# Optimization experiments

Measured on AMD Instinct MI355X. Metric: run time of the kernel, lower is better.

The kernel has to match this reference:

```python
import jax, jax.numpy as jnp
import numpy as np

H = 2048          # hidden size
NH = 32           # query heads
NKV = 8           # kv heads
HD = H // NH      # head dim = 64
GROUPS = NH // NKV
S = 2048          # seq len
B = 1
SCALE = HD ** -0.5


def _rope_tables(seq, dim, base=10000.0):
    inv = 1.0 / (base ** (np.arange(0, dim, 2, dtype=np.float32) / dim))
    t = np.arange(seq, dtype=np.float32)
    freqs = np.outer(t, inv)                     # [S, dim/2]
    emb = np.concatenate([freqs, freqs], axis=-1)  # [S, dim]
    return jnp.asarray(np.cos(emb)), jnp.asarray(np.sin(emb))


def setup_inputs() -> dict:
    key = jax.random.key(0)
    ks = jax.random.split(key, 5)
    x = jax.random.normal(ks[0], (B, S, H), dtype=jnp.float32)
    wq = jax.random.normal(ks[1], (H, NH * HD), dtype=jnp.float32) * (H ** -0.5)
    wk = jax.random.normal(ks[2], (H, NKV * HD), dtype=jnp.float32) * (H ** -0.5)
    wv = jax.random.normal(ks[3], (H, NKV * HD), dtype=jnp.float32) * (H ** -0.5)
    wo = jax.random.normal(ks[4], (NH * HD, H), dtype=jnp.float32) * (H ** -0.5)
    cos, sin = _rope_tables(S, HD)
    mask = jnp.tril(jnp.ones((S, S), dtype=bool))[None, None]  # causal [1,1,S,S]
    return {"x": x, "wq": wq, "wk": wk, "wv": wv, "wo": wo,
            "cos": cos, "sin": sin, "mask": mask}


def _rotate_half(t):
    t1, t2 = jnp.split(t, 2, axis=-1)
    return jnp.concatenate([-t2, t1], axis=-1)


def reference(x, wq, wk, wv, wo, cos, sin, mask):
    b, s, _ = x.shape
    # projections
    q = (x @ wq).reshape(b, s, NH, HD).transpose(0, 2, 1, 3)    # [B,NH,S,HD]
    k = (x @ wk).reshape(b, s, NKV, HD).transpose(0, 2, 1, 3)   # [B,NKV,S,HD]
    v = (x @ wv).reshape(b, s, NKV, HD).transpose(0, 2, 1, 3)
    # RoPE (cos/sin broadcast over batch and heads)
    c = cos[None, None]; sn = sin[None, None]
    q = q * c + _rotate_half(q) * sn
    k = k * c + _rotate_half(k) * sn
    # GQA: repeat kv heads to match query heads
    k = jnp.repeat(k, GROUPS, axis=1)                           # [B,NH,S,HD]
    v = jnp.repeat(v, GROUPS, axis=1)
    # scores + causal mask + softmax (dropout p=0 -> identity in eval)
    scores = SCALE * jnp.einsum('bhqd,bhkd->bhqk', q, k)
    scores = jnp.where(mask, scores, -jnp.inf)
    attn = jax.nn.softmax(scores, axis=-1)
    out = jnp.einsum('bhqk,bhkd->bhqd', attn, v)
    out = out.transpose(0, 2, 1, 3).reshape(b, s, NH * HD)
    return out @ wo
```

## Files before the change

### kernel.cpp

```cpp
#include <hip/hip_runtime.h>

typedef unsigned short u16;
typedef unsigned u32;
typedef u16 u16x8 __attribute__((ext_vector_type(8)));
typedef u16 u16x4 __attribute__((ext_vector_type(4)));
typedef u32 u32x4 __attribute__((ext_vector_type(4)));
typedef __bf16 bf8 __attribute__((ext_vector_type(8)));
typedef float f32x4 __attribute__((ext_vector_type(4)));
typedef float f32x16 __attribute__((ext_vector_type(16)));

__device__ __forceinline__ u16 f2b(float f) {
  unsigned u = __float_as_uint(f);
  u += 0x7FFFu + ((u >> 16) & 1u);
  return (u16)(u >> 16);
}
__device__ __forceinline__ float b2f(u16 h) {
  return __uint_as_float(((unsigned)h) << 16);
}
__device__ __forceinline__ bf8 asbf8(u16x8 v) {
  return __builtin_bit_cast(bf8, v);
}
__device__ __forceinline__ void gll16(const u16* g, u16* l) {
  __builtin_amdgcn_global_load_lds(
      (const __attribute__((address_space(1))) unsigned*)(g),
      (__attribute__((address_space(3))) unsigned*)(l), 16, 0, 0);
}
__device__ __forceinline__ u32 cvtpk(float lo, float hi) {
  u32 r;
  asm("v_cvt_pk_bf16_f32 %0, %1, %2" : "=v"(r) : "v"(lo), "v"(hi));
  return r;
}
__device__ __forceinline__ void plswap(u32& a, u32& b) {
  asm("v_permlane32_swap_b32 %0, %1" : "+v"(a), "+v"(b));
}
__device__ __forceinline__ float ex2(float x) {
  return __builtin_amdgcn_exp2f(x);
}
#define MFMA32(A,B,C) __builtin_amdgcn_mfma_f32_32x32x16_bf16(A,B,C,0,0,0)


__global__ __launch_bounds__(256) void xconv(const float* __restrict__ x,
                                             u16* __restrict__ xb) {
  int i = (blockIdx.x * 256 + threadIdx.x) * 4;
  float4 v = *(const float4*)(x + i);
  u16x4 o;
  o[0] = f2b(v.x); o[1] = f2b(v.y); o[2] = f2b(v.z); o[3] = f2b(v.w);
  *(u16x4*)(xb + i) = o;
}

__global__ __launch_bounds__(256) void wtrans(const float* __restrict__ in,
                                              u16* __restrict__ out,
                                              int N, int K) {
  __shared__ float tile[32][33];
  int tx = threadIdx.x & 31, ty = threadIdx.x >> 5;
  int n0 = blockIdx.x * 32, k0 = blockIdx.y * 32;
#pragma unroll
  for (int yy = 0; yy < 32; yy += 8)
    tile[ty + yy][tx] = in[(size_t)(k0 + ty + yy) * N + n0 + tx];
  __syncthreads();
#pragma unroll
  for (int yy = 0; yy < 32; yy += 8)
    out[(size_t)(n0 + ty + yy) * K + k0 + tx] = f2b(tile[tx][ty + yy]);
}

__global__ __launch_bounds__(256) void reduce_qkv(u16* __restrict__ p0,
                                                  const u16* __restrict__ p1,
                                                  const float* __restrict__ cs,
                                                  const float* __restrict__ sn) {
  int idx = blockIdx.x * 256 + threadIdx.x;
  int s = idx / 384, c8 = (idx % 384) * 8;
  size_t base = (size_t)s * 3072 + c8;
  if (c8 < 2560) {
    int hc = c8 & 63;
    if (hc >= 32) return;
    u16x8 a0 = *(const u16x8*)(p0 + base);
    u16x8 a1 = *(const u16x8*)(p1 + base);
    u16x8 b0 = *(const u16x8*)(p0 + base + 32);
    u16x8 b1 = *(const u16x8*)(p1 + base + 32);
    u16x8 oa, ob;
#pragma unroll
    for (int e = 0; e < 8; ++e) {
      float va = b2f(a0[e]) + b2f(a1[e]);
      float vb = b2f(b0[e]) + b2f(b1[e]);
      float c1 = cs[s * 64 + hc + e],      s1 = sn[s * 64 + hc + e];
      float c2 = cs[s * 64 + hc + 32 + e], s2 = sn[s * 64 + hc + 32 + e];
      oa[e] = f2b(va * c1 - vb * s1);
      ob[e] = f2b(vb * c2 + va * s2);
    }
    *(u16x8*)(p0 + base)      = oa;
    *(u16x8*)(p0 + base + 32) = ob;
  } else {
    u16x8 a0 = *(const u16x8*)(p0 + base);
    u16x8 a1 = *(const u16x8*)(p1 + base);
    u16x8 o;
#pragma unroll
    for (int e = 0; e < 8; ++e) o[e] = f2b(b2f(a0[e]) + b2f(a1[e]));
    *(u16x8*)(p0 + base) = o;
  }
}

__global__ __launch_bounds__(256) void reduce_out(const u16* __restrict__ p0,
                                                  const u16* __restrict__ p1,
                                                  float* __restrict__ out) {
  int idx = blockIdx.x * 256 + threadIdx.x;
  size_t base = (size_t)idx * 8;
  u16x8 a0 = *(const u16x8*)(p0 + base);
  u16x8 a1 = *(const u16x8*)(p1 + base);
  float4 lo, hi;
  lo.x = b2f(a0[0]) + b2f(a1[0]); lo.y = b2f(a0[1]) + b2f(a1[1]);
  lo.z = b2f(a0[2]) + b2f(a1[2]); lo.w = b2f(a0[3]) + b2f(a1[3]);
  hi.x = b2f(a0[4]) + b2f(a1[4]); hi.y = b2f(a0[5]) + b2f(a1[5]);
  hi.z = b2f(a0[6]) + b2f(a1[6]); hi.w = b2f(a0[7]) + b2f(a1[7]);
  *(float4*)(out + base)     = lo;
  *(float4*)(out + base + 4) = hi;
}

__global__ __launch_bounds__(256) void ktrans_f(const u16* __restrict__ qkv,
                                                u16* __restrict__ Kf) {
  int tid = blockIdx.x * 256 + threadIdx.x;
  int s = tid >> 6, cc = tid & 63;
  int kh = cc >> 3, c = cc & 7;
  int j = c >> 1, hi = c & 1;
  int b = s >> 5, la = s & 31;
  u16x8 v = *(const u16x8*)(qkv + (size_t)s * 3072 + 2048 + cc * 8);
  *(u16x8*)(Kf + ((((size_t)(kh * 64 + b) * 4 + j) * 2 + hi) * 32 + la) * 8) = v;
}

__global__ __launch_bounds__(256) void vtrans_f(const u16* __restrict__ qkv,
                                                u16* __restrict__ Vf) {
  int tid = blockIdx.x * 256 + threadIdx.x;
  int s = tid >> 6, cc = tid & 63;
  int kh = cc >> 3, c = cc & 7;
  int m = c >> 2, laB = (c & 3) * 8;
  int b = s >> 5, s5 = s & 31;
  int jj = s5 >> 4, hi = (s5 >> 3) & 1, e = s5 & 7;
  u16x8 v = *(const u16x8*)(qkv + (size_t)s * 3072 + 2560 + cc * 8);
  u16* dst = Vf + (((size_t)(kh * 64 + b) * 4 + m * 2 + jj) * 64 + hi * 32 + laB) * 8 + e;
#pragma unroll
  for (int i = 0; i < 8; ++i) dst[i * 8] = v[i];
}


__global__ __launch_bounds__(256) void gemm_sk(const u16* __restrict__ A,
                                               const u16* __restrict__ Bt,
                                               u16* __restrict__ C0,
                                               u16* __restrict__ C1,
                                               int N, int Kfull, int KH) {
  __shared__ __align__(16) u16 As[128 * 64];
  __shared__ __align__(16) u16 Bs[128 * 64];
  const int t = threadIdx.x;
  const int lane = t & 63, wid = t >> 6;
  const int wm = (wid >> 1) * 64, wn = (wid & 1) * 64;
  const int la = lane & 15, lg = lane >> 4;
  const int m0 = blockIdx.y * 128, n0 = blockIdx.x * 128;
  const int kbeg = blockIdx.z * KH;
  u16* C = blockIdx.z ? C1 : C0;

  const int srow0 = wid * 32 + (lane >> 3);
  const int scolsw = (((lane & 7) ^ (lane >> 3))) * 8;
  const u16* Ap = A + (size_t)(m0 + srow0) * Kfull + kbeg + scolsw;
  const u16* Bp = Bt + (size_t)(n0 + srow0) * Kfull + kbeg + scolsw;
  u16* Adst = &As[wid * 2048];
  u16* Bdst = &Bs[wid * 2048];
  const size_t rstep8 = (size_t)8 * Kfull;

  f32x4 acc[4][4] = {};

  for (int k0 = 0; k0 < KH; k0 += 64) {
    __syncthreads();
#pragma unroll
    for (int cc = 0; cc < 4; ++cc)
      gll16(Ap + k0 + cc * rstep8, Adst + cc * 512);
#pragma unroll
    for (int cc = 0; cc < 4; ++cc)
      gll16(Bp + k0 + cc * rstep8, Bdst + cc * 512);
    __syncthreads();
#pragma unroll
    for (int kk = 0; kk < 2; ++kk) {
      bf8 af[4], bfr[4];
#pragma unroll
      for (int i = 0; i < 4; ++i) {
        const int row = wm + i * 16 + la;
        const int c8 = (kk * 4 + lg) ^ (row & 7);
        af[i] = asbf8(*(const u16x8*)(&As[row * 64 + c8 * 8]));
      }
#pragma unroll
      for (int j = 0; j < 4; ++j) {
        const int row = wn + j * 16 + la;
        const int c8 = (kk * 4 + lg) ^ (row & 7);
        bfr[j] = asbf8(*(const u16x8*)(&Bs[row * 64 + c8 * 8]));
      }
      __builtin_amdgcn_s_setprio(1);
#pragma unroll
      for (int i = 0; i < 4; ++i)
#pragma unroll
        for (int j = 0; j < 4; ++j)
          acc[i][j] = __builtin_amdgcn_mfma_f32_16x16x32_bf16(af[i], bfr[j],
                                                              acc[i][j], 0, 0, 0);
      __builtin_amdgcn_s_setprio(0);
    }
  }

#pragma unroll
  for (int i = 0; i < 4; ++i)
#pragma unroll
    for (int j = 0; j < 4; ++j)
#pragma unroll
      for (int r = 0; r < 4; ++r) {
        int row = m0 + wm + i * 16 + lg * 4 + r;
        int col = n0 + wn + j * 16 + la;
        C[(size_t)row * N + col] = f2b(acc[i][j][r]);
      }
}


#define STEPL(buf, bb) do {                                          \
    const u16* p_ = &smem[(((h2) << 1) | (buf)) * 4096 + lane8];     \
    bf8 K0 = asbf8(*(const u16x8*)(p_));                             \
    bf8 K1 = asbf8(*(const u16x8*)(p_ + 512));                       \
    bf8 K2 = asbf8(*(const u16x8*)(p_ + 1024));                      \
    bf8 K3 = asbf8(*(const u16x8*)(p_ + 1536));                      \
    bf8 V0 = asbf8(*(const u16x8*)(p_ + 2048));                      \
    bf8 V1 = asbf8(*(const u16x8*)(p_ + 2560));                      \
    bf8 V2 = asbf8(*(const u16x8*)(p_ + 3072));                      \
    bf8 V3 = asbf8(*(const u16x8*)(p_ + 3584));                      \
    f32x16 s = {};                                                   \
    __builtin_amdgcn_s_setprio(1);                                   \
    s = MFMA32(K0, qf0, s);                                          \
    s = MFMA32(K1, qf1, s);                                          \
    s = MFMA32(K2, qf2, s);                                          \
    s = MFMA32(K3, qf3, s);                                          \
    __builtin_amdgcn_s_setprio(0);                                   \
    if ((bb) == kmax) {                                              \
      _Pragma("unroll") for (int r = 0; r < 16; ++r) {               \
        int kvr = (bb) * 32 + (r & 3) + 8 * (r >> 2) + 4 * hi;       \
        if (kvr > q0w + la) s[r] = -1e30f;                           \
      }                                                              \
    }                                                                \
    _Pragma("unroll") for (int r = 0; r < 16; ++r)                   \
      s[r] = ex2(s[r] - 32.0f);                                      \
    float z0 = s[0] + s[1],   z1 = s[2] + s[3];                      \
    float z2 = s[4] + s[5],   z3 = s[6] + s[7];                      \
    float z4 = s[8] + s[9],   z5 = s[10] + s[11];                    \
    float z6 = s[12] + s[13], z7 = s[14] + s[15];                    \
    l_run += ((z0 + z1) + (z2 + z3)) + ((z4 + z5) + (z6 + z7));      \
    u32 c0 = cvtpk(s[0], s[1]),   c1 = cvtpk(s[2], s[3]);            \
    u32 c2 = cvtpk(s[4], s[5]),   c3 = cvtpk(s[6], s[7]);            \
    u32 c4 = cvtpk(s[8], s[9]),   c5 = cvtpk(s[10], s[11]);          \
    u32 c6 = cvtpk(s[12], s[13]), c7 = cvtpk(s[14], s[15]);          \
    plswap(c0, c2); plswap(c1, c3); plswap(c4, c6); plswap(c5, c7);  \
    u32x4 t0; t0[0] = c0; t0[1] = c1; t0[2] = c2; t0[3] = c3;        \
    u32x4 t1; t1[0] = c4; t1[1] = c5; t1[2] = c6; t1[3] = c7;        \
    bf8 pa0 = __builtin_bit_cast(bf8, t0);                           \
    bf8 pa1 = __builtin_bit_cast(bf8, t1);                           \
    __builtin_amdgcn_s_setprio(1);                                   \
    o0 = MFMA32(pa0, V0, o0);                                        \
    o0 = MFMA32(pa1, V1, o0);                                        \
    o1 = MFMA32(pa0, V2, o1);                                        \
    o1 = MFMA32(pa1, V3, o1);                                        \
    __builtin_amdgcn_s_setprio(0);                                   \
  } while (0)

#define STG(bb, buf) do {                                            \
    u16* d_ = &smem[((((h2) << 1) | (buf)) * 4096) + sub * 512];     \
    gll16(Kg + (size_t)(bb) * 2048 + sub * 512 + lane8, d_);         \
    gll16(Vg + (size_t)(bb) * 2048 + sub * 512 + lane8, d_ + 2048);  \
  } while (0)

__global__ __launch_bounds__(512, 4) void attn_fwd(const u16* __restrict__ qkv,
                                                   const u16* __restrict__ Kf,
                                                   const u16* __restrict__ Vf,
                                                   u16* __restrict__ aout) {
  const int head = blockIdx.x;
  const int qb = 15 - (int)blockIdx.y;
  const int Q0 = qb * 128;
  const int Kb = qb * 4;
  const int nb = Kb + 4;
  const int ha = nb >> 1;
  const int kh = head >> 2;
  const int t = threadIdx.x;
  const int w = t >> 6, lane = t & 63;
  const int h2 = w >> 2;
  const int wq = w & 3;
  const int sub = wq;
  const int la = lane & 31;
  const int hi = lane >> 5;
  const int lane8 = lane * 8;
  const int q0w = Q0 + 32 * wq;
  const int kmax = Kb + wq;

  __shared__ __align__(16) u16 smem[18432];
  __shared__ float lM[8][32];

  bf8 qf0, qf1, qf2, qf3;
  {
    const u16* qp = qkv + (size_t)(q0w + la) * 3072 + head * 64 + hi * 8;
    const float SC = 0.125f * 1.44269504088896340736f;
#define QLOAD(dst, kk) do {                                          \
      u16x8 v = *(const u16x8*)(qp + (kk) * 16);                     \
      u16x8 sv;                                                      \
      _Pragma("unroll") for (int e = 0; e < 8; ++e)                  \
        sv[e] = f2b(b2f(v[e]) * SC);                                 \
      dst = asbf8(sv);                                               \
    } while (0)
    QLOAD(qf0, 0); QLOAD(qf1, 1); QLOAD(qf2, 2); QLOAD(qf3, 3);
#undef QLOAD
  }

  const u16* Kg = Kf + (size_t)kh * 131072;
  const u16* Vg = Vf + (size_t)kh * 131072;

  f32x16 o0 = {}, o1 = {};
  float l_run = 0.f;

  STG(h2 ? ha : 0, 0);
  __syncthreads();

  for (int i = 0; i < ha; ++i) {
    if (i + 1 < ha) STG(h2 ? (ha + i + 1) : (i + 1), (i + 1) & 1);
    const int bb = h2 ? (ha + i) : i;
    if (bb <= kmax) STEPL(i & 1, bb);
    __syncthreads();
  }

  {
    float lt = l_run + __shfl_xor(l_run, 32);
    if (lane < 32) lM[w][lane] = lt;
#pragma unroll
    for (int r = 0; r < 16; ++r) {
      int crow = (r & 3) + 8 * (r >> 2) + 4 * hi;
      smem[(w * 32 + crow) * 72 + la]      = f2b(o0[r]);
      smem[(w * 32 + crow) * 72 + la + 32] = f2b(o1[r]);
    }
  }
  __syncthreads();

#pragma unroll
  for (int it = 0; it < 2; ++it) {
    const int id = t + it * 512;
    const int q = id >> 3, d0 = (id & 7) * 8;
    const int wA = q >> 5, crow = q & 31;
    float inv = 1.0f / (lM[wA][crow] + lM[wA + 4][crow]);
    u16x8 a = *(const u16x8*)&smem[((wA)     * 32 + crow) * 72 + d0];
    u16x8 b = *(const u16x8*)&smem[((wA + 4) * 32 + crow) * 72 + d0];
    u16x8 outv;
#pragma unroll
    for (int j = 0; j < 8; ++j)
      outv[j] = f2b((b2f(a[j]) + b2f(b[j])) * inv);
    *(u16x8*)(aout + (size_t)(Q0 + q) * 2048 + head * 64 + d0) = outv;
  }
}


extern "C" void kernel_launch(void* const* d_in, const int* in_sizes, int n_in,
                              void* d_out, int out_size, void* d_ws, size_t ws_size,
                              hipStream_t stream) {
  (void)in_sizes; (void)n_in; (void)out_size; (void)ws_size;
  const float* x  = (const float*)d_in[0];
  const float* wq = (const float*)d_in[1];
  const float* wk = (const float*)d_in[2];
  const float* wv = (const float*)d_in[3];
  const float* wo = (const float*)d_in[4];
  const float* cs = (const float*)d_in[5];
  const float* sn = (const float*)d_in[6];

  u16* ws    = (u16*)d_ws;
  u16* xb    = ws;
  u16* wqkvT = ws + 4194304;
  u16* qkv   = ws + 10485760;
  u16* woT   = ws + 16777216;
  u16* ext   = ws + 20971520;
  u16* Kf    = wqkvT;
  u16* Vf    = wqkvT + 1048576;
  u16* aout  = xb;
  u16* op0   = qkv;
  u16* op1   = ext;

  xconv<<<4096, 256, 0, stream>>>(x, xb);
  wtrans<<<dim3(64, 64), 256, 0, stream>>>(wq, wqkvT, 2048, 2048);
  wtrans<<<dim3(16, 64), 256, 0, stream>>>(wk, wqkvT + (size_t)2048 * 2048, 512, 2048);
  wtrans<<<dim3(16, 64), 256, 0, stream>>>(wv, wqkvT + (size_t)2560 * 2048, 512, 2048);
  wtrans<<<dim3(64, 64), 256, 0, stream>>>(wo, woT, 2048, 2048);

  gemm_sk<<<dim3(24, 16, 2), 256, 0, stream>>>(xb, wqkvT, qkv, ext, 3072, 2048, 1024);
  reduce_qkv<<<3072, 256, 0, stream>>>(qkv, ext, cs, sn);
  ktrans_f<<<512, 256, 0, stream>>>(qkv, Kf);
  vtrans_f<<<512, 256, 0, stream>>>(qkv, Vf);
  attn_fwd<<<dim3(32, 16), 512, 0, stream>>>(qkv, Kf, Vf, aout);
  gemm_sk<<<dim3(16, 16, 2), 256, 0, stream>>>(aout, woT, op0, op1, 2048, 2048, 1024);
  reduce_out<<<2048, 256, 0, stream>>>(op0, op1, (float*)d_out);
}
```

Measured before the change: 142.6 us.

## Shrink attention blocks to 64 query rows and merge K/V transpose kernels

The attention kernel now gives each workgroup 64 query rows with 4 waves instead of 128 rows with 8 waves. This doubles the grid to 1024 blocks, which should improve load balance across the causal triangle and raise occupancy. Each wave now issues twice as many global-to-LDS loads per K/V stage. The separate K and V transpose kernels are also merged into one launch to cut launch overhead. In exchange, K/V tiles are reused across fewer query rows, so more global traffic goes to K/V.

```diff
diff --git a/kernel.cpp b/kernel.cpp
--- a/kernel.cpp
+++ b/kernel.cpp
@@ -115,29 +115,30 @@
   *(float4*)(out + base + 4) = hi;
 }
 
-__global__ __launch_bounds__(256) void ktrans_f(const u16* __restrict__ qkv,
-                                                u16* __restrict__ Kf) {
-  int tid = blockIdx.x * 256 + threadIdx.x;
-  int s = tid >> 6, cc = tid & 63;
-  int kh = cc >> 3, c = cc & 7;
-  int j = c >> 1, hi = c & 1;
-  int b = s >> 5, la = s & 31;
-  u16x8 v = *(const u16x8*)(qkv + (size_t)s * 3072 + 2048 + cc * 8);
-  *(u16x8*)(Kf + ((((size_t)(kh * 64 + b) * 4 + j) * 2 + hi) * 32 + la) * 8) = v;
-}
-
-__global__ __launch_bounds__(256) void vtrans_f(const u16* __restrict__ qkv,
-                                                u16* __restrict__ Vf) {
-  int tid = blockIdx.x * 256 + threadIdx.x;
-  int s = tid >> 6, cc = tid & 63;
-  int kh = cc >> 3, c = cc & 7;
-  int m = c >> 2, laB = (c & 3) * 8;
-  int b = s >> 5, s5 = s & 31;
-  int jj = s5 >> 4, hi = (s5 >> 3) & 1, e = s5 & 7;
-  u16x8 v = *(const u16x8*)(qkv + (size_t)s * 3072 + 2560 + cc * 8);
-  u16* dst = Vf + (((size_t)(kh * 64 + b) * 4 + m * 2 + jj) * 64 + hi * 32 + laB) * 8 + e;
-#pragma unroll
-  for (int i = 0; i < 8; ++i) dst[i * 8] = v[i];
+__global__ __launch_bounds__(256) void kvtrans_f(const u16* __restrict__ qkv,
+                                                 u16* __restrict__ Kf,
+                                                 u16* __restrict__ Vf) {
+  int bid = blockIdx.x;
+  if (bid < 512) {
+    int tid = bid * 256 + threadIdx.x;
+    int s = tid >> 6, cc = tid & 63;
+    int kh = cc >> 3, c = cc & 7;
+    int j = c >> 1, hi = c & 1;
+    int b = s >> 5, la = s & 31;
+    u16x8 v = *(const u16x8*)(qkv + (size_t)s * 3072 + 2048 + cc * 8);
+    *(u16x8*)(Kf + ((((size_t)(kh * 64 + b) * 4 + j) * 2 + hi) * 32 + la) * 8) = v;
+  } else {
+    int tid = (bid - 512) * 256 + threadIdx.x;
+    int s = tid >> 6, cc = tid & 63;
+    int kh = cc >> 3, c = cc & 7;
+    int m = c >> 2, laB = (c & 3) * 8;
+    int b = s >> 5, s5 = s & 31;
+    int jj = s5 >> 4, hi = (s5 >> 3) & 1, e = s5 & 7;
+    u16x8 v = *(const u16x8*)(qkv + (size_t)s * 3072 + 2560 + cc * 8);
+    u16* dst = Vf + (((size_t)(kh * 64 + b) * 4 + m * 2 + jj) * 64 + hi * 32 + laB) * 8 + e;
+#pragma unroll
+    for (int i = 0; i < 8; ++i) dst[i * 8] = v[i];
+  }
 }
 
 
@@ -262,35 +263,38 @@
   } while (0)
 
 #define STG(bb, buf) do {                                            \
-    u16* d_ = &smem[((((h2) << 1) | (buf)) * 4096) + sub * 512];     \
-    gll16(Kg + (size_t)(bb) * 2048 + sub * 512 + lane8, d_);         \
-    gll16(Vg + (size_t)(bb) * 2048 + sub * 512 + lane8, d_ + 2048);  \
+    u16* d_ = &smem[((((h2) << 1) | (buf)) * 4096) + wq * 1024];     \
+    const u16* kp_ = Kg + (size_t)(bb) * 2048 + wq * 1024 + lane8;   \
+    const u16* vp_ = Vg + (size_t)(bb) * 2048 + wq * 1024 + lane8;   \
+    gll16(kp_, d_);                                                  \
+    gll16(kp_ + 512, d_ + 512);                                      \
+    gll16(vp_, d_ + 2048);                                           \
+    gll16(vp_ + 512, d_ + 2560);                                     \
   } while (0)
 
-__global__ __launch_bounds__(512, 4) void attn_fwd(const u16* __restrict__ qkv,
+__global__ __launch_bounds__(256, 4) void attn_fwd(const u16* __restrict__ qkv,
                                                    const u16* __restrict__ Kf,
                                                    const u16* __restrict__ Vf,
                                                    u16* __restrict__ aout) {
   const int head = blockIdx.x;
-  const int qb = 15 - (int)blockIdx.y;
-  const int Q0 = qb * 128;
-  const int Kb = qb * 4;
-  const int nb = Kb + 4;
+  const int qt = 31 - (int)blockIdx.y;
+  const int Q0 = qt * 64;
+  const int Kb = qt * 2;
+  const int nb = Kb + 2;
   const int ha = nb >> 1;
   const int kh = head >> 2;
   const int t = threadIdx.x;
   const int w = t >> 6, lane = t & 63;
-  const int h2 = w >> 2;
-  const int wq = w & 3;
-  const int sub = wq;
+  const int h2 = w >> 1;
+  const int wq = w & 1;
   const int la = lane & 31;
   const int hi = lane >> 5;
   const int lane8 = lane * 8;
   const int q0w = Q0 + 32 * wq;
   const int kmax = Kb + wq;
 
-  __shared__ __align__(16) u16 smem[18432];
-  __shared__ float lM[8][32];
+  __shared__ __align__(16) u16 smem[16384];
+  __shared__ float lM[4][32];
 
   bf8 qf0, qf1, qf2, qf3;
   {
@@ -337,12 +341,12 @@
 
 #pragma unroll
   for (int it = 0; it < 2; ++it) {
-    const int id = t + it * 512;
+    const int id = t + it * 256;
     const int q = id >> 3, d0 = (id & 7) * 8;
     const int wA = q >> 5, crow = q & 31;
-    float inv = 1.0f / (lM[wA][crow] + lM[wA + 4][crow]);
+    float inv = 1.0f / (lM[wA][crow] + lM[wA + 2][crow]);
     u16x8 a = *(const u16x8*)&smem[((wA)     * 32 + crow) * 72 + d0];
-    u16x8 b = *(const u16x8*)&smem[((wA + 4) * 32 + crow) * 72 + d0];
+    u16x8 b = *(const u16x8*)&smem[((wA + 2) * 32 + crow) * 72 + d0];
     u16x8 outv;
 #pragma unroll
     for (int j = 0; j < 8; ++j)
@@ -384,9 +388,8 @@
 
   gemm_sk<<<dim3(24, 16, 2), 256, 0, stream>>>(xb, wqkvT, qkv, ext, 3072, 2048, 1024);
   reduce_qkv<<<3072, 256, 0, stream>>>(qkv, ext, cs, sn);
-  ktrans_f<<<512, 256, 0, stream>>>(qkv, Kf);
-  vtrans_f<<<512, 256, 0, stream>>>(qkv, Vf);
-  attn_fwd<<<dim3(32, 16), 512, 0, stream>>>(qkv, Kf, Vf, aout);
+  kvtrans_f<<<1024, 256, 0, stream>>>(qkv, Kf, Vf);
+  attn_fwd<<<dim3(32, 32), 256, 0, stream>>>(qkv, Kf, Vf, aout);
   gemm_sk<<<dim3(16, 16, 2), 256, 0, stream>>>(aout, woT, op0, op1, 2048, 2048, 1024);
   reduce_out<<<2048, 256, 0, stream>>>(op0, op1, (float*)d_out);
 }
```

After: 140.5 us. Within noise of the previous version (-1.4%).
